# Performance work log

Measured on AMD Instinct MI355X. Metric: run time of the kernel, lower is better.

Reference implementation:

```python
import jax, jax.numpy as jnp
import numpy as np

L1_WEIGHT = 0.5
SSIM_WEIGHT = 0.5
WINDOW_SIZE = 11
SIGMA = 1.5
C1 = 0.01 ** 2
C2 = 0.03 ** 2


def _gaussian_window(dtype):
    coords = jnp.arange(WINDOW_SIZE, dtype=dtype) - (WINDOW_SIZE // 2)
    g = jnp.exp(-(coords ** 2) / (2.0 * SIGMA ** 2))
    g = g / g.sum()
    return g[:, None] * g[None, :]  # (K, K)


def _depthwise_blur(x, win2d):
    # x: (B, C, H, W); depthwise conv with shared Gaussian kernel, SAME padding
    C = x.shape[1]
    kernel = jnp.broadcast_to(win2d[None, None], (C, 1, WINDOW_SIZE, WINDOW_SIZE))
    pad = WINDOW_SIZE // 2
    return jax.lax.conv_general_dilated(
        x, kernel,
        window_strides=(1, 1),
        padding=((pad, pad), (pad, pad)),
        dimension_numbers=("NCHW", "OIHW", "NCHW"),
        feature_group_count=C,
    )


def _ssim(img1, img2):
    win = _gaussian_window(img1.dtype)
    mu1 = _depthwise_blur(img1, win)
    mu2 = _depthwise_blur(img2, win)
    mu1_sq = mu1 * mu1
    mu2_sq = mu2 * mu2
    mu1_mu2 = mu1 * mu2
    sigma1_sq = _depthwise_blur(img1 * img1, win) - mu1_sq
    sigma2_sq = _depthwise_blur(img2 * img2, win) - mu2_sq
    sigma12 = _depthwise_blur(img1 * img2, win) - mu1_mu2
    ssim_map = ((2.0 * mu1_mu2 + C1) * (2.0 * sigma12 + C2)) / (
        (mu1_sq + mu2_sq + C1) * (sigma1_sq + sigma2_sq + C2)
    )
    return ssim_map.mean()


def setup_inputs() -> dict:
    key = jax.random.key(0)
    k1, k2 = jax.random.split(key)
    shape = (32, 3, 512, 512)
    warped = jax.random.uniform(k1, shape, dtype=jnp.float32)
    target = jax.random.uniform(k2, shape, dtype=jnp.float32)
    return {"warped": warped, "target": target}


def reference(warped, target):
    l1_loss = jnp.mean(jnp.abs(warped - target))
    ssim_val = _ssim(warped, target)
    ssim_loss = 1.0 - ssim_val
    total_loss = L1_WEIGHT * l1_loss + SSIM_WEIGHT * ssim_loss
    return total_loss
```

## Files before the change

### kernel.cpp

```cpp
#include <hip/hip_runtime.h>
#include <math.h>

#define IMW 512
#define IMH 512
#define NPIX (IMW * IMH)
#define NBX 8
#define NBY 16
#define NBLK (NBX * NBY * 96)
#define C1F 1.0e-4f
#define C2F 9.0e-4f
#define H2P 28
#define PITCH 336
#define FOFF 16384

typedef short s16x8 __attribute__((ext_vector_type(8)));
typedef float f32x4 __attribute__((ext_vector_type(4)));

__device__ __forceinline__ unsigned cvtpk(float a, float b) {
    unsigned r;
    asm("v_cvt_pk_bf16_f32 %0, %1, %2" : "=v"(r) : "v"(a), "v"(b));
    return r;
}
__device__ __forceinline__ unsigned bf16_rne(float f) {
    unsigned u = __builtin_bit_cast(unsigned, f);
    return (u + 0x7FFFu + ((u >> 16) & 1u)) >> 16;
}
__device__ __forceinline__ float bf16_to_f(unsigned b) {
    return __builtin_bit_cast(float, b << 16);
}
__device__ __forceinline__ void gload16(const void* g, void* l) {
    __builtin_amdgcn_global_load_lds(
        (const __attribute__((address_space(1))) void*)g,
        (__attribute__((address_space(3))) void*)l,
        16, 0, 0);
}
__device__ __forceinline__ f32x4 spl4(float v) { f32x4 r = {v, v, v, v}; return r; }

__global__ void setup_kernel(uint4* __restrict__ wtab)
{
    const int lane = threadIdx.x;
    const int lane15 = lane & 15;
    const int g = lane >> 4;
    float w[11];
    float s = 0.f;
    for (int i = 0; i < 11; ++i) {
        const float c = (float)(i - 5);
        w[i] = expf(-(c * c) / 4.5f);
        s += w[i];
    }
    for (int i = 0; i < 11; ++i) w[i] /= s;

    s16x8 bwh, bwl, avh, avl;
    #pragma unroll
    for (int e = 0; e < 8; ++e) {
        const int k = 8 * g + e;
        const int th = k - lane15 - 3;
        const float wh = (th >= 0 && th <= 10) ? w[th] : 0.f;
        const int tv = k - lane15;
        const float wvv = (tv >= 0 && tv <= 10) ? w[tv] : 0.f;
        const unsigned h1 = bf16_rne(wh);
        const unsigned l1 = bf16_rne(wh - bf16_to_f(h1));
        bwh[e] = (short)h1; bwl[e] = (short)l1;
        const unsigned h2 = bf16_rne(wvv);
        const unsigned l2 = bf16_rne(wvv - bf16_to_f(h2));
        avh[e] = (short)h2; avl[e] = (short)l2;
    }
    wtab[lane * 4 + 0] = __builtin_bit_cast(uint4, bwh);
    wtab[lane * 4 + 1] = __builtin_bit_cast(uint4, bwl);
    wtab[lane * 4 + 2] = __builtin_bit_cast(uint4, avh);
    wtab[lane * 4 + 3] = __builtin_bit_cast(uint4, avl);
}

__global__ __launch_bounds__(256)
void ssim_l1_kernel(const float* __restrict__ warped,
                    const float* __restrict__ target,
                    const uint4* __restrict__ wtab,
                    float2* __restrict__ partial)
{
    __shared__ unsigned int LDSU[8192];

    const int tid = threadIdx.x;
    const int lane = tid & 63;
    const int wv = tid >> 6;
    const int lane15 = lane & 15;
    const int g = (lane >> 4) & 3;
    const int c0 = blockIdx.x * 64;
    const int r0 = blockIdx.y * 32;
    const size_t base = (size_t)blockIdx.z * NPIX;
    char* LB = (char*)LDSU;

    {
        const char* xrow = (const char*)(warped + base);
        const char* yrow = (const char*)(target + base);
        const int cb0 = (c0 - 8) * 4;
        const int gb = 64 * wv + lane;
        #pragma unroll
        for (int i = 0; i < 4; ++i) {
            const int ck = wv + 4 * i;
            const unsigned G = (unsigned)(gb + 256 * i);
            const unsigned row = (G * 3121u) >> 16;
            const unsigned gl  = G - 21u * row;
            const int srow = min(max(r0 - 5 + (int)row, 0), IMH - 1);
            const int scolb = min(max(cb0 + (int)(gl << 4), 0), 2032);
            const size_t rb = (size_t)srow * (IMW * 4);
            gload16(xrow + rb + scolb, LB + 1024 * ck);
            gload16(yrow + rb + scolb, LB + FOFF + 1024 * ck);
        }
    }
    const s16x8 BwH = __builtin_bit_cast(s16x8, wtab[lane * 4 + 0]);
    const s16x8 BwL = __builtin_bit_cast(s16x8, wtab[lane * 4 + 1]);
    const s16x8 AvH = __builtin_bit_cast(s16x8, wtab[lane * 4 + 2]);
    const s16x8 AvL = __builtin_bit_cast(s16x8, wtab[lane * 4 + 3]);

    __syncthreads();

    const int s0 = 16 * wv + 8 * g;
    f32x4 cw0, cw1, mx0, mx1;
    #pragma unroll
    for (int e = 0; e < 4; ++e) {
        const int sA = s0 + e, sB = sA + 4;
        cw0[e] = (sA < 8 || sA > 71) ? 0.f : ((sA < 16 || sA >= 64) ? 1.f : 0.5f);
        cw1[e] = (sB < 8 || sB > 71) ? 0.f : ((sB < 16 || sB >= 64) ? 1.f : 0.5f);
        const int cA = c0 - 8 + sA, cB = c0 - 8 + sB;
        mx0[e] = ((unsigned)cA < (unsigned)IMW) ? 1.f : 0.f;
        mx1[e] = ((unsigned)cB < (unsigned)IMW) ? 1.f : 0.f;
    }
    const bool edge = (blockIdx.x == 0) || (blockIdx.x == NBX - 1) ||
                      (blockIdx.y == 0) || (blockIdx.y == NBY - 1);

    f32x4 l1v = spl4(0.f);
    f32x4 C[4][3];
    #pragma unroll
    for (int q = 0; q < 4; ++q)
        #pragma unroll
        for (int T = 0; T < 3; ++T)
            C[q][T] = spl4(0.f);

    const unsigned wb = (unsigned)(s0 * 4);
    #pragma unroll
    for (int T = 0; T < 3; ++T) {
        const int rs = 16 * T + lane15;
        const char* p = LB + rs * PITCH + wb;
        f32x4 x0 = *(const f32x4*)p;
        f32x4 x1 = *(const f32x4*)(p + 16);
        f32x4 y0 = *(const f32x4*)(p + FOFF);
        f32x4 y1 = *(const f32x4*)(p + FOFF + 16);
        if (edge) {
            const float rr = ((unsigned)(r0 - 5 + rs) < (unsigned)IMH) ? 1.f : 0.f;
            const f32x4 m0 = mx0 * spl4(rr);
            const f32x4 m1 = mx1 * spl4(rr);
            x0 *= m0; x1 *= m1; y0 *= m0; y1 *= m1;
        }

        {
            const float rmL1 = (T == 0) ? ((lane15 >= 5) ? 1.f : 0.f)
                             : (T == 1) ? 1.f
                             : ((lane15 <= 4) ? 1.f : 0.f);
            const f32x4 ad0 = __builtin_elementwise_abs(x0 - y0);
            const f32x4 ad1 = __builtin_elementwise_abs(x1 - y1);
            l1v = __builtin_elementwise_fma(cw0 * ad0 + cw1 * ad1, spl4(rmL1), l1v);
        }

        const f32x4 q2a = __builtin_elementwise_fma(x0, x0, y0 * y0);
        const f32x4 q2b = __builtin_elementwise_fma(x1, x1, y1 * y1);
        const f32x4 q3a = x0 * y0;
        const f32x4 q3b = x1 * y1;

        uint4 A0u, A1u, A2u, A3u;
        A0u.x = cvtpk(x0[0], x0[1]); A0u.y = cvtpk(x0[2], x0[3]);
        A0u.z = cvtpk(x1[0], x1[1]); A0u.w = cvtpk(x1[2], x1[3]);
        A1u.x = cvtpk(y0[0], y0[1]); A1u.y = cvtpk(y0[2], y0[3]);
        A1u.z = cvtpk(y1[0], y1[1]); A1u.w = cvtpk(y1[2], y1[3]);
        A2u.x = cvtpk(q2a[0], q2a[1]); A2u.y = cvtpk(q2a[2], q2a[3]);
        A2u.z = cvtpk(q2b[0], q2b[1]); A2u.w = cvtpk(q2b[2], q2b[3]);
        A3u.x = cvtpk(q3a[0], q3a[1]); A3u.y = cvtpk(q3a[2], q3a[3]);
        A3u.z = cvtpk(q3b[0], q3b[1]); A3u.w = cvtpk(q3b[2], q3b[3]);

        const s16x8 A0 = __builtin_bit_cast(s16x8, A0u);
        const s16x8 A1 = __builtin_bit_cast(s16x8, A1u);
        const s16x8 A2 = __builtin_bit_cast(s16x8, A2u);
        const s16x8 A3 = __builtin_bit_cast(s16x8, A3u);

        C[0][T] = __builtin_amdgcn_mfma_f32_16x16x32_bf16(A0, BwH, C[0][T], 0, 0, 0);
        C[0][T] = __builtin_amdgcn_mfma_f32_16x16x32_bf16(A0, BwL, C[0][T], 0, 0, 0);
        C[1][T] = __builtin_amdgcn_mfma_f32_16x16x32_bf16(A1, BwH, C[1][T], 0, 0, 0);
        C[1][T] = __builtin_amdgcn_mfma_f32_16x16x32_bf16(A1, BwL, C[1][T], 0, 0, 0);
        C[2][T] = __builtin_amdgcn_mfma_f32_16x16x32_bf16(A2, BwH, C[2][T], 0, 0, 0);
        C[2][T] = __builtin_amdgcn_mfma_f32_16x16x32_bf16(A2, BwL, C[2][T], 0, 0, 0);
        C[3][T] = __builtin_amdgcn_mfma_f32_16x16x32_bf16(A3, BwH, C[3][T], 0, 0, 0);
        C[3][T] = __builtin_amdgcn_mfma_f32_16x16x32_bf16(A3, BwL, C[3][T], 0, 0, 0);
    }
    __syncthreads();

    #pragma unroll
    for (int q = 0; q < 4; ++q) {
        #pragma unroll
        for (int T = 0; T < 3; ++T) {
            uint2 p;
            p.x = cvtpk(C[q][T][0], C[q][T][1]);
            p.y = cvtpk(C[q][T][2], C[q][T][3]);
            *(uint2*)&LDSU[((wv * 4 + q) * 16 + lane15) * H2P + 8 * T + 2 * g] = p;
        }
    }

    f32x4 ssv = spl4(0.f);
    #pragma unroll
    for (int rbh = 0; rbh < 2; ++rbh) {
        f32x4 V[4];
        #pragma unroll
        for (int q = 0; q < 4; ++q) {
            const uint4 br = *(const uint4*)&LDSU[((wv * 4 + q) * 16 + lane15) * H2P + 8 * rbh + 4 * g];
            const s16x8 B = __builtin_bit_cast(s16x8, br);
            f32x4 acc = spl4(0.f);
            acc = __builtin_amdgcn_mfma_f32_16x16x32_bf16(AvH, B, acc, 0, 0, 0);
            acc = __builtin_amdgcn_mfma_f32_16x16x32_bf16(AvL, B, acc, 0, 0, 0);
            V[q] = acc;
        }
        const f32x4 mu12  = V[0] * V[1];
        const f32x4 mu1sq = V[0] * V[0];
        const f32x4 mu2sq = V[1] * V[1];
        const f32x4 s12   = V[3] - mu12;
        const f32x4 ssig  = V[2] - mu1sq - mu2sq;
        const f32x4 num = (spl4(2.f) * mu12 + spl4(C1F)) * (spl4(2.f) * s12 + spl4(C2F));
        const f32x4 den = (mu1sq + mu2sq + spl4(C1F)) * (ssig + spl4(C2F));
        f32x4 r;
        r[0] = __builtin_amdgcn_rcpf(den[0]);
        r[1] = __builtin_amdgcn_rcpf(den[1]);
        r[2] = __builtin_amdgcn_rcpf(den[2]);
        r[3] = __builtin_amdgcn_rcpf(den[3]);
        ssv = __builtin_elementwise_fma(num, r, ssv);
    }

    float l1sum = (l1v[0] + l1v[1]) + (l1v[2] + l1v[3]);
    float ssum  = (ssv[0] + ssv[1]) + (ssv[2] + ssv[3]);
    #pragma unroll
    for (int off = 32; off > 0; off >>= 1) {
        l1sum += __shfl_down(l1sum, off);
        ssum  += __shfl_down(ssum,  off);
    }
    float* red = (float*)(LB + 32512);
    if (lane == 0) { red[wv] = l1sum; red[4 + wv] = ssum; }
    __syncthreads();
    if (tid == 0) {
        const float L1 = red[0] + red[1] + red[2] + red[3];
        const float SS = red[4] + red[5] + red[6] + red[7];
        const int bid = (blockIdx.z * gridDim.y + blockIdx.y) * gridDim.x + blockIdx.x;
        partial[bid] = make_float2(L1, SS);
    }
}

__global__ __launch_bounds__(256)
void reduce_kernel(const float2* __restrict__ partial, float* __restrict__ out)
{
    double l1 = 0.0, ss = 0.0;
    for (int i = threadIdx.x; i < NBLK; i += 256) {
        const float2 p = partial[i];
        l1 += (double)p.x;
        ss += (double)p.y;
    }
    #pragma unroll
    for (int off = 32; off > 0; off >>= 1) {
        l1 += __shfl_down(l1, off);
        ss += __shfl_down(ss, off);
    }
    __shared__ double red[8];
    const int wv = threadIdx.x >> 6, lane = threadIdx.x & 63;
    if (lane == 0) { red[wv] = l1; red[4 + wv] = ss; }
    __syncthreads();
    if (threadIdx.x == 0) {
        const double n = 25165824.0;
        const double L1 = (red[0] + red[1] + red[2] + red[3]) / n;
        const double SS = (red[4] + red[5] + red[6] + red[7]) / n;
        out[0] = (float)(0.5 * L1 + 0.5 * (1.0 - SS));
    }
}

extern "C" void kernel_launch(void* const* d_in, const int* in_sizes, int n_in,
                              void* d_out, int out_size, void* d_ws, size_t ws_size,
                              hipStream_t stream)
{
    const float* warped = (const float*)d_in[0];
    const float* target = (const float*)d_in[1];
    float* out = (float*)d_out;
    uint4* wtab = (uint4*)d_ws;
    float2* partial = (float2*)((char*)d_ws + 4096);

    hipLaunchKernelGGL(setup_kernel, dim3(1), dim3(64), 0, stream, wtab);
    hipLaunchKernelGGL(ssim_l1_kernel, dim3(NBX, NBY, 96), dim3(256), 0, stream,
                       warped, target, wtab, partial);
    hipLaunchKernelGGL(reduce_kernel, dim3(1), dim3(256), 0, stream, partial, out);
}
```

Measured before the change: 84.30 us.

## Double-buffer row bands in LDS to overlap global loads with MFMA blur

Replaces the single upfront load of the full 48-row tile with per-16-row-band staging into two alternating LDS buffers. The next band is fetched while the current band's horizontal-blur MFMAs run, and LDS drops from 32 KB to about 28 KB, which may allow more resident blocks. In exchange it adds a vmcnt wait and a barrier per band, and its correctness depends on buffer indexing and on the reduction scratch offset not overlapping live data.

After: 86.64 us. 2.8% more time.

```diff
diff --git a/kernel.cpp b/kernel.cpp
--- a/kernel.cpp
+++ b/kernel.cpp
@@ -11,7 +11,8 @@
 #define C2F 9.0e-4f
 #define H2P 28
 #define PITCH 336
-#define FOFF 16384
+#define BANDB 5376
+#define YOFF 10752
 
 typedef short s16x8 __attribute__((ext_vector_type(8)));
 typedef float f32x4 __attribute__((ext_vector_type(4)));
@@ -77,7 +78,7 @@
                     const uint4* __restrict__ wtab,
                     float2* __restrict__ partial)
 {
-    __shared__ unsigned int LDSU[8192];
+    __shared__ unsigned int LDSU[7176];
 
     const int tid = threadIdx.x;
     const int lane = tid & 63;
@@ -89,30 +90,31 @@
     const size_t base = (size_t)blockIdx.z * NPIX;
     char* LB = (char*)LDSU;
 
-    {
-        const char* xrow = (const char*)(warped + base);
-        const char* yrow = (const char*)(target + base);
-        const int cb0 = (c0 - 8) * 4;
-        const int gb = 64 * wv + lane;
-        #pragma unroll
-        for (int i = 0; i < 4; ++i) {
-            const int ck = wv + 4 * i;
-            const unsigned G = (unsigned)(gb + 256 * i);
-            const unsigned row = (G * 3121u) >> 16;
-            const unsigned gl  = G - 21u * row;
-            const int srow = min(max(r0 - 5 + (int)row, 0), IMH - 1);
-            const int scolb = min(max(cb0 + (int)(gl << 4), 0), 2032);
-            const size_t rb = (size_t)srow * (IMW * 4);
-            gload16(xrow + rb + scolb, LB + 1024 * ck);
-            gload16(yrow + rb + scolb, LB + FOFF + 1024 * ck);
-        }
-    }
+    const char* xrow = (const char*)(warped + base);
+    const char* yrow = (const char*)(target + base);
+    const int cb0 = (c0 - 8) * 4;
+
     const s16x8 BwH = __builtin_bit_cast(s16x8, wtab[lane * 4 + 0]);
     const s16x8 BwL = __builtin_bit_cast(s16x8, wtab[lane * 4 + 1]);
     const s16x8 AvH = __builtin_bit_cast(s16x8, wtab[lane * 4 + 2]);
     const s16x8 AvL = __builtin_bit_cast(s16x8, wtab[lane * 4 + 3]);
 
-    __syncthreads();
+    auto STAGE = [&](int t, int b) {
+        const int rbase = r0 - 5 + 16 * t;
+        #pragma unroll
+        for (int j = 0; j < 2; ++j) {
+            const int idx = tid + 256 * j;
+            if (idx < 336) {
+                const unsigned row = ((unsigned)idx * 3121u) >> 16;
+                const unsigned gl  = (unsigned)idx - 21u * row;
+                const int srow = min(max(rbase + (int)row, 0), IMH - 1);
+                const int scolb = min(max(cb0 + (int)(gl << 4), 0), 2032);
+                const size_t rb = (size_t)srow * (IMW * 4);
+                gload16(xrow + rb + scolb, LB + b * BANDB + idx * 16);
+                gload16(yrow + rb + scolb, LB + YOFF + b * BANDB + idx * 16);
+            }
+        }
+    };
 
     const int s0 = 16 * wv + 8 * g;
     f32x4 cw0, cw1, mx0, mx1;
@@ -136,15 +138,25 @@
         for (int T = 0; T < 3; ++T)
             C[q][T] = spl4(0.f);
 
+    STAGE(0, 0);
+    asm volatile("s_waitcnt vmcnt(0)" ::: "memory");
+    __builtin_amdgcn_s_barrier();
+    __builtin_amdgcn_sched_barrier(0);
+
     const unsigned wb = (unsigned)(s0 * 4);
     #pragma unroll
-    for (int T = 0; T < 3; ++T) {
-        const int rs = 16 * T + lane15;
-        const char* p = LB + rs * PITCH + wb;
+    for (int t = 0; t < 3; ++t) {
+        if (t < 2) {
+            STAGE(t + 1, (t + 1) & 1);
+            __builtin_amdgcn_sched_barrier(0);
+        }
+
+        const int rs = 16 * t + lane15;
+        const char* p = LB + (t & 1) * BANDB + lane15 * PITCH + wb;
         f32x4 x0 = *(const f32x4*)p;
         f32x4 x1 = *(const f32x4*)(p + 16);
-        f32x4 y0 = *(const f32x4*)(p + FOFF);
-        f32x4 y1 = *(const f32x4*)(p + FOFF + 16);
+        f32x4 y0 = *(const f32x4*)(p + YOFF);
+        f32x4 y1 = *(const f32x4*)(p + YOFF + 16);
         if (edge) {
             const float rr = ((unsigned)(r0 - 5 + rs) < (unsigned)IMH) ? 1.f : 0.f;
             const f32x4 m0 = mx0 * spl4(rr);
@@ -153,8 +165,8 @@
         }
 
         {
-            const float rmL1 = (T == 0) ? ((lane15 >= 5) ? 1.f : 0.f)
-                             : (T == 1) ? 1.f
+            const float rmL1 = (t == 0) ? ((lane15 >= 5) ? 1.f : 0.f)
+                             : (t == 1) ? 1.f
                              : ((lane15 <= 4) ? 1.f : 0.f);
             const f32x4 ad0 = __builtin_elementwise_abs(x0 - y0);
             const f32x4 ad1 = __builtin_elementwise_abs(x1 - y1);
@@ -181,16 +193,19 @@
         const s16x8 A2 = __builtin_bit_cast(s16x8, A2u);
         const s16x8 A3 = __builtin_bit_cast(s16x8, A3u);
 
-        C[0][T] = __builtin_amdgcn_mfma_f32_16x16x32_bf16(A0, BwH, C[0][T], 0, 0, 0);
-        C[0][T] = __builtin_amdgcn_mfma_f32_16x16x32_bf16(A0, BwL, C[0][T], 0, 0, 0);
-        C[1][T] = __builtin_amdgcn_mfma_f32_16x16x32_bf16(A1, BwH, C[1][T], 0, 0, 0);
-        C[1][T] = __builtin_amdgcn_mfma_f32_16x16x32_bf16(A1, BwL, C[1][T], 0, 0, 0);
-        C[2][T] = __builtin_amdgcn_mfma_f32_16x16x32_bf16(A2, BwH, C[2][T], 0, 0, 0);
-        C[2][T] = __builtin_amdgcn_mfma_f32_16x16x32_bf16(A2, BwL, C[2][T], 0, 0, 0);
-        C[3][T] = __builtin_amdgcn_mfma_f32_16x16x32_bf16(A3, BwH, C[3][T], 0, 0, 0);
-        C[3][T] = __builtin_amdgcn_mfma_f32_16x16x32_bf16(A3, BwL, C[3][T], 0, 0, 0);
-    }
-    __syncthreads();
+        C[0][t] = __builtin_amdgcn_mfma_f32_16x16x32_bf16(A0, BwH, C[0][t], 0, 0, 0);
+        C[0][t] = __builtin_amdgcn_mfma_f32_16x16x32_bf16(A0, BwL, C[0][t], 0, 0, 0);
+        C[1][t] = __builtin_amdgcn_mfma_f32_16x16x32_bf16(A1, BwH, C[1][t], 0, 0, 0);
+        C[1][t] = __builtin_amdgcn_mfma_f32_16x16x32_bf16(A1, BwL, C[1][t], 0, 0, 0);
+        C[2][t] = __builtin_amdgcn_mfma_f32_16x16x32_bf16(A2, BwH, C[2][t], 0, 0, 0);
+        C[2][t] = __builtin_amdgcn_mfma_f32_16x16x32_bf16(A2, BwL, C[2][t], 0, 0, 0);
+        C[3][t] = __builtin_amdgcn_mfma_f32_16x16x32_bf16(A3, BwH, C[3][t], 0, 0, 0);
+        C[3][t] = __builtin_amdgcn_mfma_f32_16x16x32_bf16(A3, BwL, C[3][t], 0, 0, 0);
+
+        asm volatile("s_waitcnt vmcnt(0)" ::: "memory");
+        __builtin_amdgcn_s_barrier();
+        __builtin_amdgcn_sched_barrier(0);
+    }
 
     #pragma unroll
     for (int q = 0; q < 4; ++q) {
@@ -238,7 +253,7 @@
         l1sum += __shfl_down(l1sum, off);
         ssum  += __shfl_down(ssum,  off);
     }
-    float* red = (float*)(LB + 32512);
+    float* red = (float*)(LB + 28672);
     if (lane == 0) { red[wv] = l1sum; red[4 + wv] = ssum; }
     __syncthreads();
     if (tid == 0) {
```
